# Kernel tuning notes

Hardware: AMD Instinct MI355X
Metric: run time of the kernel (lower is better)

## Reference

```python
import jax, jax.numpy as jnp
import numpy as np
import math

B, S, D, H = 4, 2048, 1024, 16
HD = D // H  # head_dim = 64


def setup_inputs() -> dict:
    key = jax.random.key(0)
    ks = jax.random.split(key, 12)
    inv = 1.0 / math.sqrt(D)
    inp = {
        "query": jax.random.normal(ks[0], (B, S, D), dtype=jnp.float32),
        "key": jax.random.normal(ks[1], (B, S, D), dtype=jnp.float32),
        "value": jax.random.normal(ks[2], (B, S, D), dtype=jnp.float32),
        # causal mask, broadcast over heads; guarantees no all-masked softmax rows
        "mask": jnp.tril(jnp.ones((S, S), dtype=jnp.int32))[None, None].repeat(B, axis=0),
        # linear params stored as (in, out); y = x @ W + b (same math as torch Linear)
        "Wq": jax.random.uniform(ks[3], (D, D), jnp.float32, -inv, inv),
        "bq": jax.random.uniform(ks[4], (D,), jnp.float32, -inv, inv),
        "Wk": jax.random.uniform(ks[5], (D, D), jnp.float32, -inv, inv),
        "bk": jax.random.uniform(ks[6], (D,), jnp.float32, -inv, inv),
        "Wv": jax.random.uniform(ks[7], (D, D), jnp.float32, -inv, inv),
        "bv": jax.random.uniform(ks[8], (D,), jnp.float32, -inv, inv),
        "Wo": jax.random.uniform(ks[9], (D, D), jnp.float32, -inv, inv),
        "bo": jax.random.uniform(ks[10], (D,), jnp.float32, -inv, inv),
    }
    return inp


def _split_heads(x):
    # [B, S, D] -> [B, H, S, HD]
    b, s, _ = x.shape
    return x.reshape(b, s, H, HD).transpose(0, 2, 1, 3)


def reference(query, key, value, mask, Wq, bq, Wk, bk, Wv, bv, Wo, bo):
    q = _split_heads(query @ Wq + bq)   # [B,H,S,HD]
    k = _split_heads(key @ Wk + bk)
    v = _split_heads(value @ Wv + bv)
    scores = jnp.einsum("bhqd,bhkd->bhqk", q, k)          # [B,H,S,S]
    scores = jnp.where(mask == 0, -jnp.inf, scores)
    attn = jax.nn.softmax(scores / math.sqrt(HD), axis=-1)
    attn = attn * mask.astype(attn.dtype)                  # post-softmax re-mask (as in source)
    out = jnp.einsum("bhqk,bhkd->bhqd", attn, v)           # [B,H,S,HD]
    out = out.transpose(0, 2, 1, 3).reshape(query.shape[0], -1, D)
    return out @ Wo + bo
```

## Files before the change

### kernel.cpp

```cpp
#include <hip/hip_runtime.h>

typedef __attribute__((ext_vector_type(8))) short short8;
typedef __attribute__((ext_vector_type(8))) unsigned short ushort8;
typedef __attribute__((ext_vector_type(4))) unsigned short us4;
typedef __attribute__((ext_vector_type(4))) float f32x4;
typedef __attribute__((ext_vector_type(4))) int i32x4;

#define S_LEN 2048
#define D_MODEL 1024
#define N_HEADS 16
#define HEAD_DIM 64

__device__ __forceinline__ unsigned short f2bf(float f) {
  union { float f; unsigned u; } x; x.f = f;
  unsigned r = x.u + 0x7FFFu + ((x.u >> 16) & 1u);
  return (unsigned short)(r >> 16);
}

__device__ __forceinline__ int pkbf(float a, float b) {
  union { float f; unsigned u; } x, y;
  x.f = a; y.f = b;
  return (int)__builtin_amdgcn_perm(y.u + 0x8000u, x.u + 0x8000u, 0x07060302u);
}

__global__ __launch_bounds__(256) void cvt3_kernel(const float* __restrict__ a,
                                                   const float* __restrict__ b,
                                                   const float* __restrict__ c,
                                                   unsigned short* __restrict__ oa,
                                                   unsigned short* __restrict__ ob,
                                                   unsigned short* __restrict__ oc) {
  int bid = blockIdx.x;
  const float* in = (bid < 4096) ? a : (bid < 8192 ? b : c);
  unsigned short* out = (bid < 4096) ? oa : (bid < 8192 ? ob : oc);
  int i = (bid & 4095) * 256 + threadIdx.x;
  const f32x4* in4 = (const f32x4*)in;
  f32x4 x = in4[2 * i], y = in4[2 * i + 1];
  i32x4 o;
  o[0] = pkbf(x[0], x[1]);
  o[1] = pkbf(x[2], x[3]);
  o[2] = pkbf(y[0], y[1]);
  o[3] = pkbf(y[2], y[3]);
  ((i32x4*)out)[i] = o;
}

__global__ __launch_bounds__(256) void transpose_w4(
    const float* __restrict__ Wq, const float* __restrict__ Wk,
    const float* __restrict__ Wv, const float* __restrict__ Wo,
    unsigned short* __restrict__ wqkvT, unsigned short* __restrict__ woT) {
  __shared__ float tile[64][65];
  const int z = blockIdx.z;
  const float* W = (z == 0) ? Wq : (z == 1) ? Wk : (z == 2) ? Wv : Wo;
  unsigned short* Wt = (z < 3) ? (wqkvT + (size_t)z * D_MODEL * D_MODEL) : woT;
  const int no = blockIdx.x * 64, ko = blockIdx.y * 64;
  const int tx = threadIdx.x & 63, ty = threadIdx.x >> 6;
  for (int r = ty; r < 64; r += 4)
    tile[r][tx] = W[(size_t)(ko + r) * D_MODEL + no + tx];
  __syncthreads();
  for (int r = ty; r < 64; r += 4)
    Wt[(size_t)(no + r) * D_MODEL + ko + tx] = f2bf(tile[tx][r]);
}

template <int MODE>
__global__ __launch_bounds__(256) void proj_gemm(
    const unsigned short* __restrict__ A0,
    const unsigned short* __restrict__ A1,
    const unsigned short* __restrict__ A2,
    const unsigned short* __restrict__ Bt,
    const float* __restrict__ b0p, const float* __restrict__ b1p,
    const float* __restrict__ b2p,
    void* __restrict__ o0, void* __restrict__ o1, void* __restrict__ o2,
    float qscale) {
  __shared__ __align__(16) unsigned short sm[16384];
  unsigned short* As = sm;
  unsigned short* Bs = sm + 8192;
  const int tid = threadIdx.x;
  const int wave = tid >> 6, lane = tid & 63;
  const int quad = lane >> 4, l16 = lane & 15;
  const int m0 = blockIdx.y * 128, n0 = blockIdx.x * 128;
  const int wm = (wave >> 1) * 64, wn = (wave & 1) * 64;

  const int sel = (MODE == 0) ? (n0 >> 10) : 0;
  const unsigned short* A = (MODE == 0) ? (sel == 0 ? A0 : sel == 1 ? A1 : A2) : A0;
  const float* bias = (MODE == 0) ? (sel == 0 ? b0p : sel == 1 ? b1p : b2p) : b0p;
  const float scale = (MODE == 0 && sel == 0) ? qscale : 1.0f;
  const int nb = (MODE == 0) ? (n0 & 1023) : n0;

  f32x4 acc[4][4] = {};

  int grow[4], gcol[4];
  for (int i = 0; i < 4; ++i) {
    int cid = (wave * 4 + i) * 64 + lane;
    int r = cid >> 3;
    grow[i] = r;
    gcol[i] = ((cid & 7) ^ (r & 7)) * 8;
  }

  for (int k0 = 0; k0 < D_MODEL; k0 += 64) {
#pragma unroll
    for (int i = 0; i < 4; ++i) {
      const unsigned short* g = A + (size_t)(m0 + grow[i]) * D_MODEL + k0 + gcol[i];
      __builtin_amdgcn_global_load_lds((const __attribute__((address_space(1))) void*)g,
          (__attribute__((address_space(3))) void*)(As + (wave * 4 + i) * 512), 16, 0, 0);
    }
#pragma unroll
    for (int i = 0; i < 4; ++i) {
      const unsigned short* g = Bt + (size_t)(n0 + grow[i]) * D_MODEL + k0 + gcol[i];
      __builtin_amdgcn_global_load_lds((const __attribute__((address_space(1))) void*)g,
          (__attribute__((address_space(3))) void*)(Bs + (wave * 4 + i) * 512), 16, 0, 0);
    }
    __syncthreads();
#pragma unroll
    for (int t = 0; t < 2; ++t) {
      short8 af[4], bf[4];
#pragma unroll
      for (int i = 0; i < 4; ++i) {
        int r = wm + i * 16 + l16;
        af[i] = *(const short8*)(As + r * 64 + (((t * 4 + quad) ^ (r & 7)) << 3));
      }
#pragma unroll
      for (int j = 0; j < 4; ++j) {
        int r = wn + j * 16 + l16;
        bf[j] = *(const short8*)(Bs + r * 64 + (((t * 4 + quad) ^ (r & 7)) << 3));
      }
#pragma unroll
      for (int i = 0; i < 4; ++i)
#pragma unroll
        for (int j = 0; j < 4; ++j)
          acc[i][j] = __builtin_amdgcn_mfma_f32_16x16x32_bf16(af[i], bf[j], acc[i][j], 0, 0, 0);
    }
    __syncthreads();
  }

  float bv4[4];
#pragma unroll
  for (int j = 0; j < 4; ++j) bv4[j] = bias[nb + wn + j * 16 + l16];

  if (MODE == 0) {
    if (sel < 2) {
      unsigned short* T = As + wave * 1152;
      unsigned short* out = (unsigned short*)(sel == 0 ? o0 : o1);
      const int h = (nb + wn) >> 6;
#pragma unroll
      for (int i = 0; i < 4; ++i) {
#pragma unroll
        for (int j = 0; j < 4; ++j)
#pragma unroll
          for (int r = 0; r < 4; ++r)
            T[(quad * 4 + r) * 72 + j * 16 + l16] = f2bf((acc[i][j][r] + bv4[j]) * scale);
        int m = m0 + wm + i * 16 + l16;
        int b = m >> 11, s = m & 2047;
#pragma unroll
        for (int t = 0; t < 2; ++t) {
          short8 row = *(const short8*)(T + l16 * 72 + t * 32 + quad * 8);
          *(short8*)(out + (((size_t)(b * N_HEADS + h) * S_LEN + s) << 6) + t * 32 + quad * 8) = row;
        }
      }
    } else {
      unsigned short* vt = (unsigned short*)o2;
#pragma unroll
      for (int i = 0; i < 4; ++i) {
        int m = m0 + wm + i * 16 + quad * 4;
        int b = m >> 11, s = m & 2047;
#pragma unroll
        for (int j = 0; j < 4; ++j) {
          int n = nb + wn + j * 16 + l16;
          int h = n >> 6, d = n & 63;
          us4 pv;
#pragma unroll
          for (int r = 0; r < 4; ++r) pv[r] = f2bf(acc[i][j][r] + bv4[j]);
          *(us4*)(vt + (((size_t)(b * N_HEADS + h) * 64 + d) << 11) + s) = pv;
        }
      }
    }
  } else {
    float* Tf = (float*)sm + wave * 1088;
    float* out = (float*)o0;
#pragma unroll
    for (int i = 0; i < 4; ++i) {
#pragma unroll
      for (int j = 0; j < 4; ++j)
#pragma unroll
        for (int r = 0; r < 4; ++r)
          Tf[(quad * 4 + r) * 68 + j * 16 + l16] = acc[i][j][r] + bv4[j];
      int m = m0 + wm + i * 16 + l16;
#pragma unroll
      for (int t = 0; t < 4; ++t) {
        f32x4 row = *(const f32x4*)(Tf + l16 * 68 + t * 16 + quad * 4);
        *(f32x4*)(out + (size_t)m * D_MODEL + nb + wn + t * 16 + quad * 4) = row;
      }
    }
  }
}

__global__ __launch_bounds__(256, 4) void flash_attn(
    const unsigned short* __restrict__ Qh,
    const unsigned short* __restrict__ Kh,
    const unsigned short* __restrict__ Vt,
    unsigned short* __restrict__ ctx) {
  __shared__ __align__(16) unsigned short smem[16384];
  const int tid = threadIdx.x;
  const int wave = tid >> 6, lane = tid & 63;
  const int quad = lane >> 4, l16 = lane & 15;
  const int l7 = l16 & 7;
  const int bh = blockIdx.y;
  const int t16 = (blockIdx.x + blockIdx.y + (blockIdx.y >> 4)) & 15;
  const int qi = (t16 & 1) ? (15 - (t16 >> 1)) : (t16 >> 1);
  const int q0 = qi * 128;
  const int nk = 2 * qi + 2;
  const size_t hb = (size_t)bh * (S_LEN * HEAD_DIM);
  const int srow = lane >> 3;
  const int schunk = ((lane & 7) ^ srow) * 8;

  auto stage = [&](int kt, int buf) {
    unsigned short* Kb = smem + buf * 8192;
    unsigned short* Vb = smem + buf * 8192 + 4096;
#pragma unroll
    for (int c = 0; c < 2; ++c) {
      int row = wave * 16 + c * 8 + srow;
      const unsigned short* gk = Kh + hb + (size_t)(kt * 64 + row) * 64 + schunk;
      __builtin_amdgcn_global_load_lds((const __attribute__((address_space(1))) void*)gk,
          (__attribute__((address_space(3))) void*)(Kb + (wave * 16 + c * 8) * 64), 16, 0, 0);
      const unsigned short* gv = Vt + hb + (size_t)row * S_LEN + kt * 64 + schunk;
      __builtin_amdgcn_global_load_lds((const __attribute__((address_space(1))) void*)gv,
          (__attribute__((address_space(3))) void*)(Vb + (wave * 16 + c * 8) * 64), 16, 0, 0);
    }
  };

  stage(0, 0);

  short8 qf[2][2];
#pragma unroll
  for (int s = 0; s < 2; ++s)
#pragma unroll
    for (int t = 0; t < 2; ++t)
      qf[s][t] = *(const short8*)(Qh + hb +
          (size_t)(q0 + wave * 32 + s * 16 + l16) * 64 + t * 32 + quad * 8);

  f32x4 o[4][2] = {};
  float rsum[2] = {0.f, 0.f};

  for (int kt = 0; kt < nk; ++kt) {
    __syncthreads();
    if (kt + 1 < nk) stage(kt + 1, (kt + 1) & 1);
    const unsigned short* Kb = smem + (kt & 1) * 8192;
    const unsigned short* Vb = Kb + 4096;

    if (kt * 64 > q0 + wave * 32 + 31) continue;

    f32x4 sc[2][4];
    __builtin_amdgcn_s_setprio(1);
#pragma unroll
    for (int nt = 0; nt < 4; ++nt) {
      short8 k0 = *(const short8*)(Kb + (nt * 16 + l16) * 64 + ((quad ^ l7) << 3));
      short8 k1 = *(const short8*)(Kb + (nt * 16 + l16) * 64 + (((4 + quad) ^ l7) << 3));
#pragma unroll
      for (int s = 0; s < 2; ++s) {
        f32x4 z = {};
        z = __builtin_amdgcn_mfma_f32_16x16x32_bf16(k0, qf[s][0], z, 0, 0, 0);
        sc[s][nt] = __builtin_amdgcn_mfma_f32_16x16x32_bf16(k1, qf[s][1], z, 0, 0, 0);
      }
    }
    __builtin_amdgcn_s_setprio(0);
    if (kt >= 2 * qi) {
#pragma unroll
      for (int s = 0; s < 2; ++s) {
        int qg = q0 + wave * 32 + s * 16 + l16;
#pragma unroll
        for (int nt = 0; nt < 4; ++nt) {
          int kg = kt * 64 + nt * 16 + quad * 4;
#pragma unroll
          for (int r = 0; r < 4; ++r)
            if (kg + r > qg) sc[s][nt][r] = -1e30f;
        }
      }
    }

    union { int i[4]; short8 v; } pf[2][2];
#pragma unroll
    for (int s = 0; s < 2; ++s) {
      int pk[4][2];
#pragma unroll
      for (int nt = 0; nt < 4; ++nt) {
        float p0 = exp2f(sc[s][nt][0]);
        float p1 = exp2f(sc[s][nt][1]);
        float p2 = exp2f(sc[s][nt][2]);
        float p3 = exp2f(sc[s][nt][3]);
        rsum[s] += (p0 + p1) + (p2 + p3);
        pk[nt][0] = pkbf(p0, p1);
        pk[nt][1] = pkbf(p2, p3);
      }
#pragma unroll
      for (int t = 0; t < 2; ++t) {
        int A = pk[t * 2][0], C = pk[t * 2 + 1][0];
        int B2 = pk[t * 2][1], D = pk[t * 2 + 1][1];
        asm("v_permlane32_swap_b32 %0, %1" : "+v"(A), "+v"(C));
        asm("v_permlane16_swap_b32 %0, %1" : "+v"(A), "+v"(C));
        asm("v_permlane32_swap_b32 %0, %1" : "+v"(B2), "+v"(D));
        asm("v_permlane16_swap_b32 %0, %1" : "+v"(B2), "+v"(D));
        pf[s][t].i[0] = A;
        pf[s][t].i[1] = B2;
        pf[s][t].i[2] = C;
        pf[s][t].i[3] = D;
      }
    }

    __builtin_amdgcn_s_setprio(1);
#pragma unroll
    for (int ntd = 0; ntd < 4; ++ntd) {
      short8 v0 = *(const short8*)(Vb + (ntd * 16 + l16) * 64 + ((quad ^ l7) << 3));
      short8 v1 = *(const short8*)(Vb + (ntd * 16 + l16) * 64 + (((4 + quad) ^ l7) << 3));
#pragma unroll
      for (int s = 0; s < 2; ++s) {
        o[ntd][s] = __builtin_amdgcn_mfma_f32_16x16x32_bf16(v0, pf[s][0].v, o[ntd][s], 0, 0, 0);
        o[ntd][s] = __builtin_amdgcn_mfma_f32_16x16x32_bf16(v1, pf[s][1].v, o[ntd][s], 0, 0, 0);
      }
    }
    __builtin_amdgcn_s_setprio(0);
  }

#pragma unroll
  for (int s = 0; s < 2; ++s) {
    rsum[s] += __shfl_xor(rsum[s], 16, 64);
    rsum[s] += __shfl_xor(rsum[s], 32, 64);
  }

  __syncthreads();
  unsigned short* Os = smem;
#pragma unroll
  for (int s = 0; s < 2; ++s) {
    float invl = 1.0f / rsum[s];
#pragma unroll
    for (int ntd = 0; ntd < 4; ++ntd) {
      us4 pk4;
#pragma unroll
      for (int r = 0; r < 4; ++r) pk4[r] = f2bf(o[ntd][s][r] * invl);
      *(us4*)(Os + (wave * 32 + s * 16 + l16) * 72 + ntd * 16 + quad * 4) = pk4;
    }
  }
  __syncthreads();
  const int b = bh >> 4, h = bh & 15;
#pragma unroll
  for (int it = 0; it < 4; ++it) {
    int e = it * 256 + tid;
    int row = e >> 3, c = (e & 7) * 8;
    short8 vrow = *(const short8*)(Os + row * 72 + c);
    *(short8*)(ctx + (size_t)(b * S_LEN + q0 + row) * D_MODEL + h * HEAD_DIM + c) = vrow;
  }
}

extern "C" void kernel_launch(void* const* d_in, const int* in_sizes, int n_in,
                              void* d_out, int out_size, void* d_ws, size_t ws_size,
                              hipStream_t stream) {
  (void)in_sizes; (void)n_in; (void)out_size;
  const float* q  = (const float*)d_in[0];
  const float* k  = (const float*)d_in[1];
  const float* v  = (const float*)d_in[2];
  const float* Wq = (const float*)d_in[4];
  const float* bq = (const float*)d_in[5];
  const float* Wk = (const float*)d_in[6];
  const float* bk = (const float*)d_in[7];
  const float* Wv = (const float*)d_in[8];
  const float* bv = (const float*)d_in[9];
  const float* Wo = (const float*)d_in[10];
  const float* bo = (const float*)d_in[11];
  float* out = (float*)d_out;

  if (ws_size < 109051904u) return;
  char* ws = (char*)d_ws;
  unsigned short* xq    = (unsigned short*)(ws);
  unsigned short* xk    = (unsigned short*)(ws + 16777216);
  unsigned short* xv    = (unsigned short*)(ws + 33554432);
  unsigned short* wqkvT = (unsigned short*)(ws + 50331648);
  unsigned short* woT   = (unsigned short*)(ws + 56623104);
  unsigned short* qh    = (unsigned short*)(ws + 58720256);
  unsigned short* kh    = qh + 8388608;
  unsigned short* vt    = kh + 8388608;
  unsigned short* ctx   = xq;

  cvt3_kernel<<<12288, 256, 0, stream>>>(q, k, v, xq, xk, xv);
  transpose_w4<<<dim3(16, 16, 4), 256, 0, stream>>>(Wq, Wk, Wv, Wo, wqkvT, woT);
  proj_gemm<0><<<dim3(24, 64), 256, 0, stream>>>(xq, xk, xv, wqkvT, bq, bk, bv,
                                                 qh, kh, vt, 0.125f * 1.44269504088896f);
  flash_attn<<<dim3(16, 64), 256, 0, stream>>>(qh, kh, vt, ctx);
  proj_gemm<1><<<dim3(8, 64), 256, 0, stream>>>(ctx, ctx, ctx, woT, bo, bo, bo,
                                                out, out, out, 1.0f);
}
```

Measured before the change: 375.3 us.

## Remap block indices for XCD-local L2 reuse and use raw exp2 intrinsic

```diff
diff --git a/kernel.cpp b/kernel.cpp
--- a/kernel.cpp
+++ b/kernel.cpp
@@ -76,7 +76,19 @@
   const int tid = threadIdx.x;
   const int wave = tid >> 6, lane = tid & 63;
   const int quad = lane >> 4, l16 = lane & 15;
-  const int m0 = blockIdx.y * 128, n0 = blockIdx.x * 128;
+
+  const int nlin = blockIdx.y * (MODE == 0 ? 24 : 8) + blockIdx.x;
+  const int xcd = nlin & 7;
+  const int j = nlin >> 3;
+  int bx_eff, by_eff;
+  if (MODE == 0) {
+    by_eff = xcd * 8 + ((j & 63) >> 3);
+    bx_eff = (j >> 6) * 8 + (j & 7);
+  } else {
+    by_eff = xcd * 8 + (j >> 3);
+    bx_eff = j & 7;
+  }
+  const int m0 = by_eff * 128, n0 = bx_eff * 128;
   const int wm = (wave >> 1) * 64, wn = (wave & 1) * 64;
 
   const int sel = (MODE == 0) ? (n0 >> 10) : 0;
@@ -118,22 +130,22 @@
         af[i] = *(const short8*)(As + r * 64 + (((t * 4 + quad) ^ (r & 7)) << 3));
       }
 #pragma unroll
-      for (int j = 0; j < 4; ++j) {
-        int r = wn + j * 16 + l16;
-        bf[j] = *(const short8*)(Bs + r * 64 + (((t * 4 + quad) ^ (r & 7)) << 3));
+      for (int j2 = 0; j2 < 4; ++j2) {
+        int r = wn + j2 * 16 + l16;
+        bf[j2] = *(const short8*)(Bs + r * 64 + (((t * 4 + quad) ^ (r & 7)) << 3));
       }
 #pragma unroll
       for (int i = 0; i < 4; ++i)
 #pragma unroll
-        for (int j = 0; j < 4; ++j)
-          acc[i][j] = __builtin_amdgcn_mfma_f32_16x16x32_bf16(af[i], bf[j], acc[i][j], 0, 0, 0);
+        for (int j2 = 0; j2 < 4; ++j2)
+          acc[i][j2] = __builtin_amdgcn_mfma_f32_16x16x32_bf16(af[i], bf[j2], acc[i][j2], 0, 0, 0);
     }
     __syncthreads();
   }
 
   float bv4[4];
 #pragma unroll
-  for (int j = 0; j < 4; ++j) bv4[j] = bias[nb + wn + j * 16 + l16];
+  for (int j2 = 0; j2 < 4; ++j2) bv4[j2] = bias[nb + wn + j2 * 16 + l16];
 
   if (MODE == 0) {
     if (sel < 2) {
@@ -143,10 +155,10 @@
 #pragma unroll
       for (int i = 0; i < 4; ++i) {
 #pragma unroll
-        for (int j = 0; j < 4; ++j)
+        for (int j2 = 0; j2 < 4; ++j2)
 #pragma unroll
           for (int r = 0; r < 4; ++r)
-            T[(quad * 4 + r) * 72 + j * 16 + l16] = f2bf((acc[i][j][r] + bv4[j]) * scale);
+            T[(quad * 4 + r) * 72 + j2 * 16 + l16] = f2bf((acc[i][j2][r] + bv4[j2]) * scale);
         int m = m0 + wm + i * 16 + l16;
         int b = m >> 11, s = m & 2047;
 #pragma unroll
@@ -162,12 +174,12 @@
         int m = m0 + wm + i * 16 + quad * 4;
         int b = m >> 11, s = m & 2047;
 #pragma unroll
-        for (int j = 0; j < 4; ++j) {
-          int n = nb + wn + j * 16 + l16;
+        for (int j2 = 0; j2 < 4; ++j2) {
+          int n = nb + wn + j2 * 16 + l16;
           int h = n >> 6, d = n & 63;
           us4 pv;
 #pragma unroll
-          for (int r = 0; r < 4; ++r) pv[r] = f2bf(acc[i][j][r] + bv4[j]);
+          for (int r = 0; r < 4; ++r) pv[r] = f2bf(acc[i][j2][r] + bv4[j2]);
           *(us4*)(vt + (((size_t)(b * N_HEADS + h) * 64 + d) << 11) + s) = pv;
         }
       }
@@ -178,10 +190,10 @@
 #pragma unroll
     for (int i = 0; i < 4; ++i) {
 #pragma unroll
-      for (int j = 0; j < 4; ++j)
+      for (int j2 = 0; j2 < 4; ++j2)
 #pragma unroll
         for (int r = 0; r < 4; ++r)
-          Tf[(quad * 4 + r) * 68 + j * 16 + l16] = acc[i][j][r] + bv4[j];
+          Tf[(quad * 4 + r) * 68 + j2 * 16 + l16] = acc[i][j2][r] + bv4[j2];
       int m = m0 + wm + i * 16 + l16;
 #pragma unroll
       for (int t = 0; t < 4; ++t) {
@@ -202,9 +214,15 @@
   const int wave = tid >> 6, lane = tid & 63;
   const int quad = lane >> 4, l16 = lane & 15;
   const int l7 = l16 & 7;
-  const int bh = blockIdx.y;
-  const int t16 = (blockIdx.x + blockIdx.y + (blockIdx.y >> 4)) & 15;
-  const int qi = (t16 & 1) ? (15 - (t16 >> 1)) : (t16 >> 1);
+
+  const int nlin = blockIdx.y * 16 + blockIdx.x;
+  const int xcd = nlin & 7;
+  const int rr = nlin >> 3;
+  const int bh = xcd * 8 + (rr & 7);
+  const int qslot = rr >> 3;
+  const int qa = qslot & 3, qb = qslot >> 2;
+  const int qbase = qa + ((qb >> 1) << 2);
+  const int qi = (qb & 1) ? (15 - qbase) : qbase;
   const int q0 = qi * 128;
   const int nk = 2 * qi + 2;
   const size_t hb = (size_t)bh * (S_LEN * HEAD_DIM);
@@ -281,10 +299,10 @@
       int pk[4][2];
 #pragma unroll
       for (int nt = 0; nt < 4; ++nt) {
-        float p0 = exp2f(sc[s][nt][0]);
-        float p1 = exp2f(sc[s][nt][1]);
-        float p2 = exp2f(sc[s][nt][2]);
-        float p3 = exp2f(sc[s][nt][3]);
+        float p0 = __builtin_amdgcn_exp2f(sc[s][nt][0]);
+        float p1 = __builtin_amdgcn_exp2f(sc[s][nt][1]);
+        float p2 = __builtin_amdgcn_exp2f(sc[s][nt][2]);
+        float p3 = __builtin_amdgcn_exp2f(sc[s][nt][3]);
         rsum[s] += (p0 + p1) + (p2 + p3);
         pk[nt][0] = pkbf(p0, p1);
         pk[nt][1] = pkbf(p2, p3);
```

Measured after the change: 328.9 us. -12.4%, faster.
